# Performance work log

Measured on AMD Instinct MI355X. Metric: run time of the kernel, lower is better.

## Reference

```python
import jax, jax.numpy as jnp
import numpy as np

B, N = 8, 48
NEMBED, EMBED_DIM, HID_DIM = 1000, 32, 32
IN_DIM = EMBED_DIM + 1  # feature dim after concatenating xfeat
N_OPS = 8  # exchangeable 3-tensor basis: identity + means over each nonempty axis subset


def setup_inputs() -> dict:
    key = jax.random.key(0)
    k1, k2, k3, k4, k5 = jax.random.split(key, 5)
    xcat = jax.random.randint(k1, (B, N), 0, NEMBED)
    xfeat = jax.random.normal(k2, (B, N), dtype=jnp.float32)
    embed_table = jax.random.normal(k3, (NEMBED, EMBED_DIM), dtype=jnp.float32)
    # SetEq3to3 coefficients: (in_dim, n_basis_ops, out_dim), Glorot-ish scale
    coefs = jax.random.normal(k4, (IN_DIM, N_OPS, HID_DIM), dtype=jnp.float32) * np.sqrt(2.0 / (IN_DIM + HID_DIM))
    eq_bias = jnp.zeros((HID_DIM,), dtype=jnp.float32)
    out_w = jax.random.normal(k5, (HID_DIM, 1), dtype=jnp.float32) * np.sqrt(1.0 / HID_DIM)
    out_b = jnp.zeros((1,), dtype=jnp.float32)
    return {"xcat": xcat, "xfeat": xfeat, "embed_table": embed_table,
            "coefs": coefs, "eq_bias": eq_bias, "out_w": out_w, "out_b": out_b}


def _set_eq3to3(t, coefs, eq_bias):
    # t: (B, d, n, n, n); coefs: (d, 8, h). Each basis op is a mean over a
    # subset of the three set axes (kept as size-1 dims so broadcasting restores shape).
    def mix(op, s):
        return jnp.einsum('bd...,dh->bh...', op, coefs[:, s, :])
    m_i = t.mean(axis=2, keepdims=True)
    m_j = t.mean(axis=3, keepdims=True)
    m_k = t.mean(axis=4, keepdims=True)
    m_ij = m_i.mean(axis=3, keepdims=True)
    m_ik = m_i.mean(axis=4, keepdims=True)
    m_jk = m_j.mean(axis=4, keepdims=True)
    m_ijk = m_ij.mean(axis=4, keepdims=True)
    out = (mix(t, 0) + mix(m_i, 1) + mix(m_j, 2) + mix(m_k, 3)
           + mix(m_ij, 4) + mix(m_ik, 5) + mix(m_jk, 6) + mix(m_ijk, 7))
    return out + eq_bias.reshape(1, -1, 1, 1, 1)  # (B, h, n, n, n)


def reference(xcat, xfeat, embed_table, coefs, eq_bias, out_w, out_b):
    e = embed_table[xcat]                                   # (B, n, d_e)
    x = jnp.concatenate([e, xfeat[..., None]], axis=-1)      # (B, n, d) with d = d_e + 1
    t = jnp.einsum('bid,bjd,bkd->bdijk', x, x, x)            # (B, d, n, n, n)
    y = _set_eq3to3(t, coefs, eq_bias)                       # (B, h, n, n, n)
    y = jnp.transpose(y, (0, 2, 3, 4, 1))                    # (B, n, n, n, h)
    y = jax.nn.relu(y)
    y = y.mean(axis=(1, 2, 3))                               # (B, h) mean pool
    y = jax.nn.relu(y)
    # dropout is inactive in eval mode (training=False)
    return y @ out_w + out_b                                 # (B, 1)
```

## Files before the change

kernel.cpp:

```cpp
#include <hip/hip_runtime.h>
#include <cstdint>
#include <cstddef>

#define BB 8
#define NN 48
#define DD 33
#define XS 40
#define KP 128
#define HH 32
#define MM (NN*NN)
#define NC (NN*HH)
#define TILE 96
#define TM (MM/TILE)
#define TN (NC/TILE)
#define NBLK (TM*TN)
#define LDK 136

typedef __attribute__((ext_vector_type(8))) _Float16 f16x8;
typedef __attribute__((ext_vector_type(4))) float f32x4;

__global__ void k_setup(const int* __restrict__ xcat, const float* __restrict__ xfeat,
                        const float* __restrict__ embed, const float* __restrict__ coefs,
                        const float* __restrict__ eq_bias,
                        float* __restrict__ xw, float* __restrict__ sw,
                        float* __restrict__ ct, float* __restrict__ gk) {
    int b = blockIdx.x, t = threadIdx.x;
    __shared__ float sl[XS];
    if (b < BB) {
        for (int idx = t; idx < NN * XS; idx += 256) {
            int i = idx / XS, d = idx - i * XS;
            float v = 0.f;
            if (d < 32)       v = embed[xcat[b * NN + i] * 32 + d];
            else if (d == 32) v = xfeat[b * NN + i];
            xw[b * NN * XS + idx] = v;
        }
        __syncthreads();
        if (t < XS) {
            float a = 0.f;
            for (int i = 0; i < NN; ++i) a += xw[b * NN * XS + i * XS + t];
            float s = a * (1.0f / 48.0f);
            sw[b * XS + t] = s;
            sl[t] = s;
        }
        __syncthreads();
        for (int idx = t; idx < NC; idx += 256) {
            int k = idx >> 5, h = idx & 31;
            const float* xk = xw + (b * NN + k) * XS;
            float g = 0.f;
            for (int d = 0; d < DD; ++d) {
                float sd = sl[d];
                g += sd * sd * (coefs[(d * 8 + 4) * HH + h] * xk[d]
                              + coefs[(d * 8 + 7) * HH + h] * sd);
            }
            gk[b * NC + idx] = g + eq_bias[h];
        }
    } else {
        for (int idx = t; idx < 8 * HH * XS; idx += 256) {
            int qh = idx / XS, d = idx - qh * XS;
            int q = qh >> 5, h = qh & 31;
            ct[idx] = (d < DD) ? coefs[(d * 8 + q) * HH + h] : 0.f;
        }
    }
}

__global__ __launch_bounds__(256, 3) void k_gemm(
        const float* __restrict__ xw, const float* __restrict__ sw,
        const float* __restrict__ ct, const float* __restrict__ gk,
        float* __restrict__ partials) {
    __shared__ __align__(16) _Float16 As[TILE][LDK];
    __shared__ __align__(16) _Float16 Bs[TILE][LDK];
    __shared__ float hacc[HH];

    int t = threadIdx.x;
    int bx = blockIdx.x, by = blockIdx.y, b = blockIdx.z;
    int N0 = bx * TILE, M0 = by * TILE;
    const float* xb = xw + b * NN * XS;
    const float* sb = sw + b * XS;

    if (t < HH) hacc[t] = 0.f;

    for (int c = 0; c < 6; ++c) {
        int ch = c * 256 + t;
        int row = ch >> 4, d0 = (ch & 15) * 8;
        {
            int n = N0 + row, k = n >> 5, h = n & 31;
            const float* xk = xb + k * XS;
            f16x8 v;
            if (d0 < 120) {
                int seg = (d0 >= 80) ? 2 : (d0 >= 40) ? 1 : 0;
                int d = d0 - seg * 40;
                const int QA[3] = {0, 2, 1}, QB[3] = {3, 6, 5};
                const float* ca = ct + (QA[seg] * HH + h) * XS + d;
                const float* cb = ct + (QB[seg] * HH + h) * XS + d;
                f32x4 ca0 = *(const f32x4*)(ca),     ca1 = *(const f32x4*)(ca + 4);
                f32x4 cb0 = *(const f32x4*)(cb),     cb1 = *(const f32x4*)(cb + 4);
                f32x4 xk0 = *(const f32x4*)(xk + d), xk1 = *(const f32x4*)(xk + d + 4);
                f32x4 sb0 = *(const f32x4*)(sb + d), sb1 = *(const f32x4*)(sb + d + 4);
                f32x4 r0 = ca0 * xk0 + cb0 * sb0;
                f32x4 r1 = ca1 * xk1 + cb1 * sb1;
                for (int e = 0; e < 4; ++e) { v[e] = (_Float16)r0[e]; v[4 + e] = (_Float16)r1[e]; }
            } else {
                v = (f16x8){0, 0, 0, 0, 0, 0, 0, 0};
                v[0] = (_Float16)gk[b * NC + N0 + row];
            }
            *(f16x8*)&Bs[row][d0] = v;
        }
        {
            int grow = M0 + row;
            int i = grow / NN, j = grow - i * NN;
            f16x8 v;
            if (d0 < 120) {
                int seg = (d0 >= 80) ? 2 : (d0 >= 40) ? 1 : 0;
                int d = d0 - seg * 40;
                const float* p1 = (seg == 2) ? (xb + j * XS) : (xb + i * XS);
                const float* p2 = (seg == 0) ? (xb + j * XS) : sb;
                f32x4 a0 = *(const f32x4*)(p1 + d), a1 = *(const f32x4*)(p1 + d + 4);
                f32x4 b0 = *(const f32x4*)(p2 + d), b1 = *(const f32x4*)(p2 + d + 4);
                f32x4 r0 = a0 * b0, r1 = a1 * b1;
                for (int e = 0; e < 4; ++e) { v[e] = (_Float16)r0[e]; v[4 + e] = (_Float16)r1[e]; }
            } else {
                v = (f16x8){0, 0, 0, 0, 0, 0, 0, 0};
                v[0] = (_Float16)1.f;
            }
            *(f16x8*)&As[row][d0] = v;
        }
    }
    __syncthreads();

    int lane = t & 63, wave = t >> 6;
    int wm = (wave >> 1) * 48, wn = (wave & 1) * 48;
    int lrow = lane & 15, quad = lane >> 4;

    f32x4 acc[3][3];
#pragma unroll
    for (int m3 = 0; m3 < 3; ++m3)
#pragma unroll
        for (int nt = 0; nt < 3; ++nt)
            acc[m3][nt] = (f32x4){0.f, 0.f, 0.f, 0.f};

#pragma unroll
    for (int ks = 0; ks < 4; ++ks) {
        f16x8 af[3], bf[3];
#pragma unroll
        for (int m3 = 0; m3 < 3; ++m3)
            af[m3] = *(const f16x8*)&As[wm + m3 * 16 + lrow][ks * 32 + quad * 8];
#pragma unroll
        for (int nt = 0; nt < 3; ++nt)
            bf[nt] = *(const f16x8*)&Bs[wn + nt * 16 + lrow][ks * 32 + quad * 8];
#pragma unroll
        for (int m3 = 0; m3 < 3; ++m3)
#pragma unroll
            for (int nt = 0; nt < 3; ++nt)
                acc[m3][nt] = __builtin_amdgcn_mfma_f32_16x16x32_f16(af[m3], bf[nt], acc[m3][nt], 0, 0, 0);
    }

    float fs[3] = {0.f, 0.f, 0.f};
#pragma unroll
    for (int m3 = 0; m3 < 3; ++m3)
#pragma unroll
        for (int nt = 0; nt < 3; ++nt)
#pragma unroll
            for (int r = 0; r < 4; ++r)
                fs[nt] += fmaxf(acc[m3][nt][r], 0.f);

#pragma unroll
    for (int nt = 0; nt < 3; ++nt) {
        float v = fs[nt];
        v += __shfl_xor(v, 16);
        v += __shfl_xor(v, 32);
        if (lane < 16) atomicAdd(&hacc[(wn + nt * 16 + lane) & 31], v);
    }
    __syncthreads();
    if (t < HH) {
        int blockLin = by * TN + bx;
        partials[((size_t)b * NBLK + blockLin) * HH + t] = hacc[t];
    }
}

__global__ void k_final(const float* __restrict__ partials, const float* __restrict__ out_w,
                        const float* __restrict__ out_b, float* __restrict__ out) {
    __shared__ float red[256];
    int b = blockIdx.x, t = threadIdx.x;
    int h = t & 31, g = t >> 5;
    float a = 0.f;
    for (int p = g; p < NBLK; p += 8) a += partials[((size_t)b * NBLK + p) * HH + h];
    red[t] = a;
    __syncthreads();
    if (t < HH) {
        float tot = 0.f;
        for (int gg = 0; gg < 8; ++gg) tot += red[gg * 32 + t];
        float m = tot * (1.0f / 110592.0f);
        red[t] = fmaxf(m, 0.f) * out_w[t];
    }
    __syncthreads();
    if (t == 0) {
        float o = 0.f;
        for (int h2 = 0; h2 < HH; ++h2) o += red[h2];
        out[b] = o + out_b[0];
    }
}

extern "C" void kernel_launch(void* const* d_in, const int* in_sizes, int n_in,
                              void* d_out, int out_size, void* d_ws, size_t ws_size,
                              hipStream_t stream) {
    (void)in_sizes; (void)n_in; (void)out_size; (void)ws_size;
    const int*   xcat    = (const int*)d_in[0];
    const float* xfeat   = (const float*)d_in[1];
    const float* embed   = (const float*)d_in[2];
    const float* coefs   = (const float*)d_in[3];
    const float* eq_bias = (const float*)d_in[4];
    const float* out_w   = (const float*)d_in[5];
    const float* out_b   = (const float*)d_in[6];
    float* out = (float*)d_out;

    char* w = (char*)d_ws;
    float* xw       = (float*)(w + 0);
    float* sw       = (float*)(w + 61440);
    float* ct       = (float*)(w + 62720);
    float* gk       = (float*)(w + 103680);
    float* partials = (float*)(w + 152832);

    k_setup<<<dim3(BB + 1), dim3(256), 0, stream>>>(xcat, xfeat, embed, coefs, eq_bias,
                                                    xw, sw, ct, gk);
    k_gemm<<<dim3(TN, TM, BB), dim3(256), 0, stream>>>(xw, sw, ct, gk, partials);
    k_final<<<dim3(BB), dim3(256), 0, stream>>>(partials, out_w, out_b, out);
}
```

Before: 131.6 us.

## Materialize fp16 GEMM operands in a separate build kernel before the GEMM

Adds a k_build kernel that computes the fp16 A (pairwise products) and B (coefficient-mixed) operand matrices once into workspace, so the GEMM only copies precomputed tiles into LDS. In the old code every GEMM block recomputed its A and B tiles, so the same tiles were rebuilt many times across the grid. The change adds an extra launch and roughly 8 MB of global writes and reads in exchange for removing that repeated operand construction.

```diff
diff --git a/kernel.cpp b/kernel.cpp
--- a/kernel.cpp
+++ b/kernel.cpp
@@ -15,6 +15,8 @@
 #define TN (NC/TILE)
 #define NBLK (TM*TN)
 #define LDK 136
+#define ABLK (BB*MM/16)
+#define BBLK (BB*NC/16)
 
 typedef __attribute__((ext_vector_type(8))) _Float16 f16x8;
 typedef __attribute__((ext_vector_type(4))) float f32x4;
@@ -63,9 +65,64 @@
     }
 }
 
-__global__ __launch_bounds__(256, 3) void k_gemm(
+__global__ __launch_bounds__(256) void k_build(
         const float* __restrict__ xw, const float* __restrict__ sw,
         const float* __restrict__ ct, const float* __restrict__ gk,
+        _Float16* __restrict__ Aw, _Float16* __restrict__ Bw) {
+    int t = threadIdx.x, blk = blockIdx.x;
+    if (blk < ABLK) {
+        int g = blk * 256 + t;
+        int row = g >> 4, d0 = (g & 15) * 8;
+        int b = row / MM, grow = row - b * MM;
+        int i = grow / NN, j = grow - i * NN;
+        const float* xb = xw + b * NN * XS;
+        const float* sb = sw + b * XS;
+        f16x8 v;
+        if (d0 < 120) {
+            int seg = (d0 >= 80) ? 2 : (d0 >= 40) ? 1 : 0;
+            int d = d0 - seg * 40;
+            const float* p1 = (seg == 2) ? (xb + j * XS) : (xb + i * XS);
+            const float* p2 = (seg == 0) ? (xb + j * XS) : sb;
+            f32x4 a0 = *(const f32x4*)(p1 + d), a1 = *(const f32x4*)(p1 + d + 4);
+            f32x4 b0 = *(const f32x4*)(p2 + d), b1 = *(const f32x4*)(p2 + d + 4);
+            f32x4 r0 = a0 * b0, r1 = a1 * b1;
+            for (int e = 0; e < 4; ++e) { v[e] = (_Float16)r0[e]; v[4 + e] = (_Float16)r1[e]; }
+        } else {
+            v = (f16x8){0, 0, 0, 0, 0, 0, 0, 0};
+            v[0] = (_Float16)1.f;
+        }
+        *(f16x8*)&Aw[(size_t)row * KP + d0] = v;
+    } else {
+        int g = (blk - ABLK) * 256 + t;
+        int row = g >> 4, d0 = (g & 15) * 8;
+        int b = row / NC, n = row - b * NC;
+        int k = n >> 5, h = n & 31;
+        const float* xk = xw + (b * NN + k) * XS;
+        const float* sb = sw + b * XS;
+        f16x8 v;
+        if (d0 < 120) {
+            int seg = (d0 >= 80) ? 2 : (d0 >= 40) ? 1 : 0;
+            int d = d0 - seg * 40;
+            const int QA[3] = {0, 2, 1}, QB[3] = {3, 6, 5};
+            const float* ca = ct + (QA[seg] * HH + h) * XS + d;
+            const float* cb = ct + (QB[seg] * HH + h) * XS + d;
+            f32x4 ca0 = *(const f32x4*)(ca),     ca1 = *(const f32x4*)(ca + 4);
+            f32x4 cb0 = *(const f32x4*)(cb),     cb1 = *(const f32x4*)(cb + 4);
+            f32x4 xk0 = *(const f32x4*)(xk + d), xk1 = *(const f32x4*)(xk + d + 4);
+            f32x4 sb0 = *(const f32x4*)(sb + d), sb1 = *(const f32x4*)(sb + d + 4);
+            f32x4 r0 = ca0 * xk0 + cb0 * sb0;
+            f32x4 r1 = ca1 * xk1 + cb1 * sb1;
+            for (int e = 0; e < 4; ++e) { v[e] = (_Float16)r0[e]; v[4 + e] = (_Float16)r1[e]; }
+        } else {
+            v = (f16x8){0, 0, 0, 0, 0, 0, 0, 0};
+            v[0] = (_Float16)gk[b * NC + n];
+        }
+        *(f16x8*)&Bw[(size_t)row * KP + d0] = v;
+    }
+}
+
+__global__ __launch_bounds__(256, 3) void k_gemm(
+        const _Float16* __restrict__ Aw, const _Float16* __restrict__ Bw,
         float* __restrict__ partials) {
     __shared__ __align__(16) _Float16 As[TILE][LDK];
     __shared__ __align__(16) _Float16 Bs[TILE][LDK];
@@ -74,56 +131,19 @@
     int t = threadIdx.x;
     int bx = blockIdx.x, by = blockIdx.y, b = blockIdx.z;
     int N0 = bx * TILE, M0 = by * TILE;
-    const float* xb = xw + b * NN * XS;
-    const float* sb = sw + b * XS;
+    const _Float16* Ag = Aw + ((size_t)(b * MM + M0)) * KP;
+    const _Float16* Bg = Bw + ((size_t)(b * NC + N0)) * KP;
 
     if (t < HH) hacc[t] = 0.f;
 
+#pragma unroll
     for (int c = 0; c < 6; ++c) {
         int ch = c * 256 + t;
         int row = ch >> 4, d0 = (ch & 15) * 8;
-        {
-            int n = N0 + row, k = n >> 5, h = n & 31;
-            const float* xk = xb + k * XS;
-            f16x8 v;
-            if (d0 < 120) {
-                int seg = (d0 >= 80) ? 2 : (d0 >= 40) ? 1 : 0;
-                int d = d0 - seg * 40;
-                const int QA[3] = {0, 2, 1}, QB[3] = {3, 6, 5};
-                const float* ca = ct + (QA[seg] * HH + h) * XS + d;
-                const float* cb = ct + (QB[seg] * HH + h) * XS + d;
-                f32x4 ca0 = *(const f32x4*)(ca),     ca1 = *(const f32x4*)(ca + 4);
-                f32x4 cb0 = *(const f32x4*)(cb),     cb1 = *(const f32x4*)(cb + 4);
-                f32x4 xk0 = *(const f32x4*)(xk + d), xk1 = *(const f32x4*)(xk + d + 4);
-                f32x4 sb0 = *(const f32x4*)(sb + d), sb1 = *(const f32x4*)(sb + d + 4);
-                f32x4 r0 = ca0 * xk0 + cb0 * sb0;
-                f32x4 r1 = ca1 * xk1 + cb1 * sb1;
-                for (int e = 0; e < 4; ++e) { v[e] = (_Float16)r0[e]; v[4 + e] = (_Float16)r1[e]; }
-            } else {
-                v = (f16x8){0, 0, 0, 0, 0, 0, 0, 0};
-                v[0] = (_Float16)gk[b * NC + N0 + row];
-            }
-            *(f16x8*)&Bs[row][d0] = v;
-        }
-        {
-            int grow = M0 + row;
-            int i = grow / NN, j = grow - i * NN;
-            f16x8 v;
-            if (d0 < 120) {
-                int seg = (d0 >= 80) ? 2 : (d0 >= 40) ? 1 : 0;
-                int d = d0 - seg * 40;
-                const float* p1 = (seg == 2) ? (xb + j * XS) : (xb + i * XS);
-                const float* p2 = (seg == 0) ? (xb + j * XS) : sb;
-                f32x4 a0 = *(const f32x4*)(p1 + d), a1 = *(const f32x4*)(p1 + d + 4);
-                f32x4 b0 = *(const f32x4*)(p2 + d), b1 = *(const f32x4*)(p2 + d + 4);
-                f32x4 r0 = a0 * b0, r1 = a1 * b1;
-                for (int e = 0; e < 4; ++e) { v[e] = (_Float16)r0[e]; v[4 + e] = (_Float16)r1[e]; }
-            } else {
-                v = (f16x8){0, 0, 0, 0, 0, 0, 0, 0};
-                v[0] = (_Float16)1.f;
-            }
-            *(f16x8*)&As[row][d0] = v;
-        }
+        f16x8 va = *(const f16x8*)(Ag + row * KP + d0);
+        f16x8 vb = *(const f16x8*)(Bg + row * KP + d0);
+        *(f16x8*)&As[row][d0] = va;
+        *(f16x8*)&Bs[row][d0] = vb;
     }
     __syncthreads();
 
@@ -214,14 +234,17 @@
     float* out = (float*)d_out;
 
     char* w = (char*)d_ws;
-    float* xw       = (float*)(w + 0);
-    float* sw       = (float*)(w + 61440);
-    float* ct       = (float*)(w + 62720);
-    float* gk       = (float*)(w + 103680);
-    float* partials = (float*)(w + 152832);
+    float*    xw       = (float*)(w + 0);
+    float*    sw       = (float*)(w + 61440);
+    float*    ct       = (float*)(w + 62720);
+    float*    gk       = (float*)(w + 103680);
+    _Float16* Aw       = (_Float16*)(w + 152832);
+    _Float16* Bw       = (_Float16*)(w + 4871424);
+    float*    partials = (float*)(w + 8017152);
 
     k_setup<<<dim3(BB + 1), dim3(256), 0, stream>>>(xcat, xfeat, embed, coefs, eq_bias,
                                                     xw, sw, ct, gk);
-    k_gemm<<<dim3(TN, TM, BB), dim3(256), 0, stream>>>(xw, sw, ct, gk, partials);
+    k_build<<<dim3(ABLK + BBLK), dim3(256), 0, stream>>>(xw, sw, ct, gk, Aw, Bw);
+    k_gemm<<<dim3(TN, TM, BB), dim3(256), 0, stream>>>(Aw, Bw, partials);
     k_final<<<dim3(BB), dim3(256), 0, stream>>>(partials, out_w, out_b, out);
 }
```

New measurement: 108.7 us. -17.4%, faster.
